# Performance work log

Hardware: AMD Instinct MI355X
Metric: run time of the kernel (lower is better)

Reference implementation:

```python
import jax, jax.numpy as jnp
import numpy as np

N_NODES = 100000
N_EDGES = 1600000
IN_CH = 128
OUT_CH = 64
HID = 2 * OUT_CH  # 128


def setup_inputs() -> dict:
    key = jax.random.key(0)
    ks = jax.random.split(key, 8)
    x = jax.random.normal(ks[0], (N_NODES, IN_CH), dtype=jnp.float32)
    edge_index = jax.random.randint(ks[1], (2, N_EDGES), 0, N_NODES, dtype=jnp.int64)

    def glorot(k, shape):
        return jax.random.normal(k, shape, dtype=jnp.float32) / jnp.sqrt(jnp.float32(shape[0]))

    W1 = glorot(ks[2], (IN_CH, HID))
    b1 = jax.random.normal(ks[3], (HID,), dtype=jnp.float32) * 0.01
    W_mu = glorot(ks[4], (HID, OUT_CH))
    b_mu = jax.random.normal(ks[5], (OUT_CH,), dtype=jnp.float32) * 0.01
    W_logstd = glorot(ks[6], (HID, OUT_CH))
    b_logstd = jax.random.normal(ks[7], (OUT_CH,), dtype=jnp.float32) * 0.01
    return {"x": x, "edge_index": edge_index, "W1": W1, "b1": b1,
            "W_mu": W_mu, "b_mu": b_mu, "W_logstd": W_logstd, "b_logstd": b_logstd}


def _gcn_norm(edge_index, n_nodes):
    # PyG GCNConv: add self-loops, symmetric normalization deg^{-1/2} A deg^{-1/2}
    loop = jnp.arange(n_nodes, dtype=edge_index.dtype)
    src = jnp.concatenate([edge_index[0], loop])  # [E+N]
    dst = jnp.concatenate([edge_index[1], loop])  # [E+N]
    deg = jax.ops.segment_sum(jnp.ones_like(dst, dtype=jnp.float32), dst,
                              num_segments=n_nodes)
    dinv = jnp.where(deg > 0, jax.lax.rsqrt(jnp.maximum(deg, 1.0)), 0.0)
    norm = dinv[src] * dinv[dst]  # [E+N]
    return src, dst, norm


def _gcn_conv(x, src, dst, norm, W, b, n_nodes):
    h = x @ W                                   # [N, out] linear first (small out dims)
    msg = h[src] * norm[:, None]                # [E+N, out] gather + scale
    out = jax.ops.segment_sum(msg, dst, num_segments=n_nodes)  # scatter-add
    return out + b


def reference(x, edge_index, W1, b1, W_mu, b_mu, W_logstd, b_logstd):
    n = x.shape[0]
    src, dst, norm = _gcn_norm(edge_index, n)  # same graph for all three layers
    h = jax.nn.relu(_gcn_conv(x, src, dst, norm, W1, b1, n))
    mu = _gcn_conv(h, src, dst, norm, W_mu, b_mu, n)
    logstd = _gcn_conv(h, src, dst, norm, W_logstd, b_logstd, n)
    return mu, logstd
```

## Files before the change

kernel.cpp:

```cpp
#include <hip/hip_runtime.h>
#include <stdint.h>

#define N_NODES 100000
#define N_EDGES 1600000
#define BSHIFT 9
#define NB 196
#define CAP 9216

typedef __attribute__((ext_vector_type(8))) short short8;
typedef __attribute__((ext_vector_type(4))) float f32x4;
typedef __attribute__((ext_vector_type(2))) float f32x2;
typedef __attribute__((ext_vector_type(4))) unsigned u32x4;
typedef __attribute__((ext_vector_type(2))) unsigned u32x2;
typedef __attribute__((ext_vector_type(4))) int i32x4;

static __device__ __forceinline__ unsigned short f2bf(float f){
  unsigned u = __float_as_uint(f);
  u += 0x7fffu + ((u >> 16) & 1u);
  return (unsigned short)(u >> 16);
}
static __device__ __forceinline__ unsigned pack2bf(float a, float b){
  return (unsigned)f2bf(a) | ((unsigned)f2bf(b) << 16);
}

__global__ __launch_bounds__(256)
void k_init(const float* __restrict__ W1, const float* __restrict__ Wmu,
            const float* __restrict__ Wls, short8* __restrict__ img,
            unsigned* __restrict__ gcur){
  int t = threadIdx.x;
  if (blockIdx.x == 16){
    if (t < NB) gcur[t] = t * CAP;
    return;
  }
  int gid = blockIdx.x*256 + t;
  int k = gid >> 11, slot = gid & 2047;
  int lane = slot & 63, ks = (slot >> 6) & 3, tt = slot >> 8;
  int c = tt*16 + (lane & 15);
  int kb = ks*32 + (lane >> 4)*8;
  short8 v;
  #pragma unroll
  for (int j = 0; j < 8; ++j){
    float f;
    if (k == 0) f = W1[(kb + j)*128 + c];
    else        f = (c < 64) ? Wmu[(kb + j)*64 + c] : Wls[(kb + j)*64 + (c - 64)];
    v[j] = (short)f2bf(f);
  }
  img[gid] = v;
}

__global__ __launch_bounds__(256)
void k_binB(const int* __restrict__ ei, unsigned* __restrict__ gcur,
            unsigned* __restrict__ tmp){
  __shared__ unsigned cnt[NB];
  __shared__ unsigned base[NB];
  int t = threadIdx.x;
  for (int j = t; j < NB; j += 256) cnt[j] = 0u;
  __syncthreads();
  unsigned bk[8], rk[8], en[8];
  int e0 = blockIdx.x*2048 + t*8;
  #pragma unroll
  for (int half = 0; half < 2; ++half){
    i32x4 sv, dv;
    bool any = (e0 + half*4) < N_EDGES;
    if (any){
      sv = *(const i32x4*)(ei + e0 + half*4);
      dv = *(const i32x4*)(ei + N_EDGES + e0 + half*4);
    }
    #pragma unroll
    for (int j = 0; j < 4; ++j){
      int q = half*4 + j;
      int e = e0 + q;
      bool ok = e < N_EDGES;
      unsigned d = ok ? (unsigned)dv[j] : 0u;
      unsigned s = ok ? (unsigned)sv[j] : 0u;
      ok = ok && d < N_NODES && s < N_NODES;
      bk[q] = ok ? (d >> BSHIFT) : 0xffffffffu;
      rk[q] = 0u; en[q] = 0u;
      if (ok){ rk[q] = atomicAdd(&cnt[bk[q]], 1u); en[q] = s | ((d & 511u) << 17); }
    }
  }
  __syncthreads();
  for (int j = t; j < NB; j += 256)
    base[j] = cnt[j] ? atomicAdd(&gcur[j], cnt[j]) : 0u;
  __syncthreads();
  #pragma unroll
  for (int j = 0; j < 8; ++j)
    if (bk[j] != 0xffffffffu){
      unsigned p = base[bk[j]] + rk[j];
      if (p < (bk[j] + 1u)*CAP) tmp[p] = en[j];
    }
}

__global__ __launch_bounds__(256)
void k_binC(const unsigned* __restrict__ gcur, const unsigned* __restrict__ tmp,
            unsigned* __restrict__ csr, unsigned* __restrict__ begdeg,
            float* __restrict__ dinv){
  __shared__ unsigned cnt[512];
  __shared__ unsigned cur[512];
  __shared__ unsigned sc[512];
  int b = blockIdx.x, t = threadIdx.x;
  unsigned base = (unsigned)b * CAP;
  unsigned sz = min(gcur[b] - base, (unsigned)CAP);
  cnt[t] = 0u; cnt[t + 256] = 0u;
  __syncthreads();
  for (unsigned idx = t; idx < sz; idx += 256){
    unsigned en = tmp[base + idx];
    atomicAdd(&cnt[(en >> 17) & 511u], 1u);
  }
  __syncthreads();
  sc[t] = cnt[t]; sc[t + 256] = cnt[t + 256];
  __syncthreads();
  for (int off = 1; off < 512; off <<= 1){
    unsigned a0 = (t >= off)       ? sc[t - off]       : 0u;
    unsigned a1 = (t + 256 >= off) ? sc[t + 256 - off] : 0u;
    __syncthreads();
    sc[t] += a0; sc[t + 256] += a1;
    __syncthreads();
  }
  {
    unsigned e0 = sc[t] - cnt[t], e1 = sc[t + 256] - cnt[t + 256];
    cur[t] = e0; cur[t + 256] = e1;
    int n0 = b*512 + t, n1 = b*512 + t + 256;
    if (n0 < N_NODES){
      begdeg[n0] = ((base + e0) << 11) | cnt[t];
      dinv[n0] = rsqrtf((float)(cnt[t] + 1u));
    }
    if (n1 < N_NODES){
      begdeg[n1] = ((base + e1) << 11) | cnt[t + 256];
      dinv[n1] = rsqrtf((float)(cnt[t + 256] + 1u));
    }
  }
  __syncthreads();
  for (unsigned idx = t; idx < sz; idx += 256){
    unsigned en = tmp[base + idx];
    unsigned p = atomicAdd(&cur[(en >> 17) & 511u], 1u);
    csr[base + p] = en;
  }
}

__global__ __launch_bounds__(256)
void k_pack(const unsigned* __restrict__ csr, const float* __restrict__ dinv,
            u32x2* __restrict__ csr2){
  int e = blockIdx.x*256 + threadIdx.x;
  if (e >= NB*CAP) return;
  unsigned src = csr[e] & 0x1FFFFu;
  src = min(src, (unsigned)(N_NODES - 1));
  u32x2 v; v[0] = src; v[1] = __float_as_uint(dinv[src]);
  csr2[e] = v;
}

template<bool AF32>
__global__ __launch_bounds__(256)
void k_gemm(const void* __restrict__ A_, const short8* __restrict__ img,
            unsigned short* __restrict__ out, int M)
{
  __shared__ short8 wf[2048];
  int tid = threadIdx.x;
  #pragma unroll
  for (int s = 0; s < 8; ++s) wf[tid + 256*s] = img[tid + 256*s];
  __syncthreads();

  int wave = tid >> 6, lane = tid & 63;
  int rb = blockIdx.x*128 + wave*32;
  int r0 = rb + (lane & 15);
  int r1 = r0 + 16;
  int ra0 = min(r0, M-1), ra1 = min(r1, M-1);
  int koff = (lane >> 4)*8;

  short8 a0[4], a1[4];
  if (AF32){
    const float* A = (const float*)A_;
    #pragma unroll
    for (int ks = 0; ks < 4; ++ks){
      const float* p0 = A + (size_t)ra0*128 + ks*32 + koff;
      const float* p1 = A + (size_t)ra1*128 + ks*32 + koff;
      f32x4 xa = *(const f32x4*)p0, xb = *(const f32x4*)(p0 + 4);
      f32x4 ya = *(const f32x4*)p1, yb = *(const f32x4*)(p1 + 4);
      short8 t0, t1;
      #pragma unroll
      for (int j = 0; j < 4; ++j){
        t0[j] = (short)f2bf(xa[j]); t0[j+4] = (short)f2bf(xb[j]);
        t1[j] = (short)f2bf(ya[j]); t1[j+4] = (short)f2bf(yb[j]);
      }
      a0[ks] = t0; a1[ks] = t1;
    }
  } else {
    const unsigned short* A = (const unsigned short*)A_;
    #pragma unroll
    for (int ks = 0; ks < 4; ++ks){
      a0[ks] = *(const short8*)(A + (size_t)ra0*128 + ks*32 + koff);
      a1[ks] = *(const short8*)(A + (size_t)ra1*128 + ks*32 + koff);
    }
  }

  f32x4 acc[2][8];
  #pragma unroll
  for (int t = 0; t < 8; ++t){ acc[0][t] = (f32x4)0.f; acc[1][t] = (f32x4)0.f; }

  #pragma unroll
  for (int t = 0; t < 8; ++t){
    #pragma unroll
    for (int ks = 0; ks < 4; ++ks){
      short8 b = wf[(t*4 + ks)*64 + lane];
      acc[0][t] = __builtin_amdgcn_mfma_f32_16x16x32_bf16(a0[ks], b, acc[0][t], 0, 0, 0);
      acc[1][t] = __builtin_amdgcn_mfma_f32_16x16x32_bf16(a1[ks], b, acc[1][t], 0, 0, 0);
    }
  }

  #pragma unroll
  for (int sub = 0; sub < 2; ++sub){
    int rbase = rb + sub*16 + (lane >> 4)*4;
    int c = lane & 15;
    #pragma unroll
    for (int t = 0; t < 8; ++t){
      #pragma unroll
      for (int j = 0; j < 4; ++j){
        int r = rbase + j;
        if (r < M) out[(size_t)r*128 + t*16 + c] = f2bf(acc[sub][t][j]);
      }
    }
  }
}

template<int MODE>
__global__ __launch_bounds__(256)
void k_agg(const unsigned short* __restrict__ hin, const unsigned* __restrict__ begdeg,
           const u32x2* __restrict__ csr2, const float* __restrict__ dinv,
           const float* __restrict__ bias, const float* __restrict__ bias2,
           unsigned* __restrict__ out_bf, float* __restrict__ out_f)
{
  int i = blockIdx.x*4 + (threadIdx.x >> 6);
  int lane = threadIdx.x & 63;
  int slot = lane >> 4, c8 = lane & 15;
  float di = dinv[i];

  f32x2 acc2[4];
  {
    u32x4 sv = *(const u32x4*)(hin + (size_t)i*128 + c8*8);
    float ws = (slot == 0) ? di*di : 0.f;
    #pragma unroll
    for (int j = 0; j < 4; ++j){
      f32x2 v; v.x = __uint_as_float(sv[j] << 16); v.y = __uint_as_float(sv[j] & 0xffff0000u);
      acc2[j].x = ws * v.x; acc2[j].y = ws * v.y;
    }
  }

  unsigned pk = begdeg[i];
  unsigned beg = pk >> 11, end = beg + (pk & 2047u);
  int nit = ((int)(pk & 2047u) + 7) >> 3;

  u32x2 fall; fall[0] = (unsigned)i; fall[1] = 0u;
  auto ldent = [&](int it, u32x2& e0, u32x2& e1){
    unsigned p0 = beg + (unsigned)(it*8) + (unsigned)(2*slot);
    unsigned p1 = p0 + 1;
    u32x2 t0 = csr2[p0 < end ? p0 : beg];
    u32x2 t1 = csr2[p1 < end ? p1 : beg];
    e0 = (p0 < end) ? t0 : fall;
    e1 = (p1 < end) ? t1 : fall;
  };

  u32x2 eA0, eA1, eB0, eB1;
  ldent(0, eA0, eA1);
  ldent(1, eB0, eB1);
  float    wA0 = di * __uint_as_float(eA0[1]), wA1 = di * __uint_as_float(eA1[1]);
  unsigned sA0 = eA0[0], sA1 = eA1[0];
  u32x4 rA0 = *(const u32x4*)(hin + (size_t)sA0*128 + c8*8);
  u32x4 rA1 = *(const u32x4*)(hin + (size_t)sA1*128 + c8*8);
  float    wB0 = di * __uint_as_float(eB0[1]), wB1 = di * __uint_as_float(eB1[1]);
  unsigned sB0 = eB0[0], sB1 = eB1[0];

  for (int it = 0; it < nit; ++it){
    u32x2 eC0, eC1;
    ldent(it + 2, eC0, eC1);
    u32x4 rB0 = *(const u32x4*)(hin + (size_t)sB0*128 + c8*8);
    u32x4 rB1 = *(const u32x4*)(hin + (size_t)sB1*128 + c8*8);

    f32x2 w0v; w0v.x = wA0; w0v.y = wA0;
    f32x2 w1v; w1v.x = wA1; w1v.y = wA1;
    #pragma unroll
    for (int j = 0; j < 4; ++j){
      f32x2 v0; v0.x = __uint_as_float(rA0[j] << 16); v0.y = __uint_as_float(rA0[j] & 0xffff0000u);
      f32x2 v1; v1.x = __uint_as_float(rA1[j] << 16); v1.y = __uint_as_float(rA1[j] & 0xffff0000u);
      acc2[j] = __builtin_elementwise_fma(w0v, v0, acc2[j]);
      acc2[j] = __builtin_elementwise_fma(w1v, v1, acc2[j]);
    }

    wA0 = wB0; wA1 = wB1; rA0 = rB0; rA1 = rB1;
    wB0 = di * __uint_as_float(eC0[1]); sB0 = eC0[0];
    wB1 = di * __uint_as_float(eC1[1]); sB1 = eC1[0];
  }

  #pragma unroll
  for (int j = 0; j < 4; ++j){
    acc2[j].x += __shfl_xor(acc2[j].x, 16);
    acc2[j].x += __shfl_xor(acc2[j].x, 32);
    acc2[j].y += __shfl_xor(acc2[j].y, 16);
    acc2[j].y += __shfl_xor(acc2[j].y, 32);
  }

  if (slot != 0) return;
  int c0 = c8*8;
  if (MODE == 0){
    u32x4 o;
    #pragma unroll
    for (int j = 0; j < 4; ++j){
      float lo = fmaxf(acc2[j].x + bias[c0 + 2*j],     0.f);
      float hi = fmaxf(acc2[j].y + bias[c0 + 2*j + 1], 0.f);
      o[j] = pack2bf(lo, hi);
    }
    *(u32x4*)(out_bf + (size_t)i*64 + c8*4) = o;
  } else {
    const float* bsrc = (c8 < 8) ? (bias + c0) : (bias2 + (c0 - 64));
    float* base = (c8 < 8) ? (out_f + (size_t)i*64 + c0)
                           : (out_f + (size_t)N_NODES*64 + (size_t)i*64 + (c0 - 64));
    f32x4 o0, o1;
    o0[0] = acc2[0].x + bsrc[0]; o0[1] = acc2[0].y + bsrc[1];
    o0[2] = acc2[1].x + bsrc[2]; o0[3] = acc2[1].y + bsrc[3];
    o1[0] = acc2[2].x + bsrc[4]; o1[1] = acc2[2].y + bsrc[5];
    o1[2] = acc2[3].x + bsrc[6]; o1[3] = acc2[3].y + bsrc[7];
    __builtin_nontemporal_store(o0, (f32x4*)base);
    __builtin_nontemporal_store(o1, (f32x4*)(base + 4));
  }
}


extern "C" void kernel_launch(void* const* d_in, const int* in_sizes, int n_in,
                              void* d_out, int out_size, void* d_ws, size_t ws_size,
                              hipStream_t stream)
{
  const float* x   = (const float*)d_in[0];
  const int*   ei  = (const int*)d_in[1];
  const float* W1  = (const float*)d_in[2];
  const float* b1  = (const float*)d_in[3];
  const float* Wmu = (const float*)d_in[4];
  const float* bmu = (const float*)d_in[5];
  const float* Wls = (const float*)d_in[6];
  const float* bls = (const float*)d_in[7];
  float* out = (float*)d_out;

  char* ws = (char*)d_ws;
  unsigned*       begdeg = (unsigned*)ws;        ws += 400128;
  float*          dinv   = (float*)ws;           ws += 400128;
  unsigned*       gcur   = (unsigned*)ws;        ws += 1024;
  short8*         imgW   = (short8*)ws;          ws += 65536;
  unsigned*       tmp    = (unsigned*)ws;        ws += 7225344;
  unsigned*       csr    = (unsigned*)ws;        ws += 7225344;
  u32x2*          csr2   = (u32x2*)ws;           ws += 14450688 + 256;
  unsigned short* bufA   = (unsigned short*)ws;  ws += 25600000;
  if (ws_size < (size_t)(ws - (char*)d_ws)) return;
  unsigned* bufB = (unsigned*)d_out;

  k_init<<<17, 256, 0, stream>>>(W1, Wmu, Wls, imgW, gcur);
  k_binB<<<(N_EDGES + 2047)/2048, 256, 0, stream>>>(ei, gcur, tmp);
  k_binC<<<NB, 256, 0, stream>>>(gcur, tmp, csr, begdeg, dinv);
  k_pack<<<(NB*CAP + 255)/256, 256, 0, stream>>>(csr, dinv, csr2);

  k_gemm<true ><<<(N_NODES + 127)/128, 256, 0, stream>>>(x, imgW, bufA, N_NODES);
  k_agg<0><<<N_NODES/4, 256, 0, stream>>>(bufA, begdeg, csr2, dinv, b1, nullptr,
                                          bufB, nullptr);
  k_gemm<false><<<(N_NODES + 127)/128, 256, 0, stream>>>((unsigned short*)bufB, imgW + 2048,
                                                         bufA, N_NODES);
  k_agg<1><<<N_NODES/4, 256, 0, stream>>>(bufA, begdeg, csr2, dinv, bmu, bls,
                                          nullptr, out);
}
```

Baseline: 218.9 us.

## Pad CSR rows to multiples of eight and stage bin scatter through LDS

Each node's CSR segment is padded to a multiple of 8 entries with zero-weight sentinel entries, so the aggregation kernel can read edge pairs as aligned 16-byte vector loads without bounds checks or fallback selects. In k_binB, edges are first grouped by bucket in shared memory with a local prefix scan, so the global scatter into tmp goes out in contiguous runs. The tmp buffer now shares memory with bufA to save workspace. The cost is a larger packed CSR (CAPP > CAP), padded entries that still gather row 0 with zero weight, and extra scan and sync work in the binning kernel.

Measured after the change: 220.1 us. No clear change (+0.6%).

```diff
diff --git a/kernel.cpp b/kernel.cpp
--- a/kernel.cpp
+++ b/kernel.cpp
@@ -5,7 +5,9 @@
 #define N_EDGES 1600000
 #define BSHIFT 9
 #define NB 196
-#define CAP 9216
+#define CAP_T 9216
+#define CAPP 11264
+#define SENT 0x80000000u
 
 typedef __attribute__((ext_vector_type(8))) short short8;
 typedef __attribute__((ext_vector_type(4))) float f32x4;
@@ -29,7 +31,7 @@
             unsigned* __restrict__ gcur){
   int t = threadIdx.x;
   if (blockIdx.x == 16){
-    if (t < NB) gcur[t] = t * CAP;
+    if (t < NB) gcur[t] = t * CAP_T;
     return;
   }
   int gid = blockIdx.x*256 + t;
@@ -52,7 +54,11 @@
 void k_binB(const int* __restrict__ ei, unsigned* __restrict__ gcur,
             unsigned* __restrict__ tmp){
   __shared__ unsigned cnt[NB];
-  __shared__ unsigned base[NB];
+  __shared__ unsigned gbase[NB];
+  __shared__ unsigned loff[NB];
+  __shared__ unsigned sc[256];
+  __shared__ unsigned sen[2048];
+  __shared__ unsigned spos[2048];
   int t = threadIdx.x;
   for (int j = t; j < NB; j += 256) cnt[j] = 0u;
   __syncthreads();
@@ -80,15 +86,33 @@
     }
   }
   __syncthreads();
-  for (int j = t; j < NB; j += 256)
-    base[j] = cnt[j] ? atomicAdd(&gcur[j], cnt[j]) : 0u;
-  __syncthreads();
+  sc[t] = (t < NB) ? cnt[t] : 0u;
+  __syncthreads();
+  for (int off = 1; off < 256; off <<= 1){
+    unsigned a = (t >= off) ? sc[t - off] : 0u;
+    __syncthreads();
+    sc[t] += a;
+    __syncthreads();
+  }
+  if (t < NB){
+    loff[t]  = sc[t] - cnt[t];
+    gbase[t] = cnt[t] ? atomicAdd(&gcur[t], cnt[t]) : 0u;
+  }
+  __syncthreads();
+  unsigned total = sc[NB - 1];
   #pragma unroll
   for (int j = 0; j < 8; ++j)
     if (bk[j] != 0xffffffffu){
-      unsigned p = base[bk[j]] + rk[j];
-      if (p < (bk[j] + 1u)*CAP) tmp[p] = en[j];
-    }
+      unsigned lp = loff[bk[j]] + rk[j];
+      unsigned gp = gbase[bk[j]] + rk[j];
+      sen[lp]  = en[j];
+      spos[lp] = (gp < (bk[j] + 1u)*CAP_T) ? gp : 0xffffffffu;
+    }
+  __syncthreads();
+  for (unsigned idx = t; idx < total; idx += 256){
+    unsigned p = spos[idx];
+    if (p != 0xffffffffu) tmp[p] = sen[idx];
+  }
 }
 
 __global__ __launch_bounds__(256)
@@ -99,16 +123,17 @@
   __shared__ unsigned cur[512];
   __shared__ unsigned sc[512];
   int b = blockIdx.x, t = threadIdx.x;
-  unsigned base = (unsigned)b * CAP;
-  unsigned sz = min(gcur[b] - base, (unsigned)CAP);
+  unsigned base_t = (unsigned)b * CAP_T;
+  unsigned basep  = (unsigned)b * CAPP;
+  unsigned sz = min(gcur[b] - base_t, (unsigned)CAP_T);
   cnt[t] = 0u; cnt[t + 256] = 0u;
   __syncthreads();
-  for (unsigned idx = t; idx < sz; idx += 256){
-    unsigned en = tmp[base + idx];
-    atomicAdd(&cnt[(en >> 17) & 511u], 1u);
-  }
-  __syncthreads();
-  sc[t] = cnt[t]; sc[t + 256] = cnt[t + 256];
+  for (unsigned idx = t; idx < sz; idx += 256)
+    atomicAdd(&cnt[(tmp[base_t + idx] >> 17) & 511u], 1u);
+  __syncthreads();
+  unsigned c0 = cnt[t], c1 = cnt[t + 256];
+  unsigned p0 = (c0 + 7u) & ~7u, p1 = (c1 + 7u) & ~7u;
+  sc[t] = p0; sc[t + 256] = p1;
   __syncthreads();
   for (int off = 1; off < 512; off <<= 1){
     unsigned a0 = (t >= off)       ? sc[t - off]       : 0u;
@@ -117,35 +142,41 @@
     sc[t] += a0; sc[t + 256] += a1;
     __syncthreads();
   }
+  unsigned e0 = sc[t] - p0, e1 = sc[t + 256] - p1;
+  cur[t] = e0; cur[t + 256] = e1;
   {
-    unsigned e0 = sc[t] - cnt[t], e1 = sc[t + 256] - cnt[t + 256];
-    cur[t] = e0; cur[t + 256] = e1;
-    int n0 = b*512 + t, n1 = b*512 + t + 256;
+    int n0 = b*512 + t, n1 = n0 + 256;
     if (n0 < N_NODES){
-      begdeg[n0] = ((base + e0) << 11) | cnt[t];
-      dinv[n0] = rsqrtf((float)(cnt[t] + 1u));
+      begdeg[n0] = (((basep + e0) >> 3) << 11) | min(c0, 2047u);
+      dinv[n0] = rsqrtf((float)(c0 + 1u));
+      for (unsigned k = c0; k < p0; ++k) csr[basep + e0 + k] = SENT;
     }
     if (n1 < N_NODES){
-      begdeg[n1] = ((base + e1) << 11) | cnt[t + 256];
-      dinv[n1] = rsqrtf((float)(cnt[t + 256] + 1u));
+      begdeg[n1] = (((basep + e1) >> 3) << 11) | min(c1, 2047u);
+      dinv[n1] = rsqrtf((float)(c1 + 1u));
+      for (unsigned k = c1; k < p1; ++k) csr[basep + e1 + k] = SENT;
     }
   }
   __syncthreads();
   for (unsigned idx = t; idx < sz; idx += 256){
-    unsigned en = tmp[base + idx];
+    unsigned en = tmp[base_t + idx];
     unsigned p = atomicAdd(&cur[(en >> 17) & 511u], 1u);
-    csr[base + p] = en;
+    if (p < (unsigned)CAPP) csr[basep + p] = en;
   }
 }
 
 __global__ __launch_bounds__(256)
 void k_pack(const unsigned* __restrict__ csr, const float* __restrict__ dinv,
             u32x2* __restrict__ csr2){
-  int e = blockIdx.x*256 + threadIdx.x;
-  if (e >= NB*CAP) return;
-  unsigned src = csr[e] & 0x1FFFFu;
-  src = min(src, (unsigned)(N_NODES - 1));
-  u32x2 v; v[0] = src; v[1] = __float_as_uint(dinv[src]);
+  unsigned e = blockIdx.x*256 + threadIdx.x;
+  if (e >= (unsigned)NB*CAPP) return;
+  unsigned en = csr[e];
+  u32x2 v;
+  if (en & SENT){ v[0] = 0u; v[1] = 0u; }
+  else {
+    unsigned src = min(en & 0x1FFFFu, (unsigned)(N_NODES - 1));
+    v[0] = src; v[1] = __float_as_uint(dinv[src]);
+  }
   csr2[e] = v;
 }
 
@@ -240,43 +271,28 @@
     float ws = (slot == 0) ? di*di : 0.f;
     #pragma unroll
     for (int j = 0; j < 4; ++j){
-      f32x2 v; v.x = __uint_as_float(sv[j] << 16); v.y = __uint_as_float(sv[j] & 0xffff0000u);
-      acc2[j].x = ws * v.x; acc2[j].y = ws * v.y;
+      acc2[j].x = ws * __uint_as_float(sv[j] << 16);
+      acc2[j].y = ws * __uint_as_float(sv[j] & 0xffff0000u);
     }
   }
 
   unsigned pk = begdeg[i];
-  unsigned beg = pk >> 11, end = beg + (pk & 2047u);
+  unsigned beg = (pk >> 11) << 3;
   int nit = ((int)(pk & 2047u) + 7) >> 3;
 
-  u32x2 fall; fall[0] = (unsigned)i; fall[1] = 0u;
-  auto ldent = [&](int it, u32x2& e0, u32x2& e1){
-    unsigned p0 = beg + (unsigned)(it*8) + (unsigned)(2*slot);
-    unsigned p1 = p0 + 1;
-    u32x2 t0 = csr2[p0 < end ? p0 : beg];
-    u32x2 t1 = csr2[p1 < end ? p1 : beg];
-    e0 = (p0 < end) ? t0 : fall;
-    e1 = (p1 < end) ? t1 : fall;
-  };
-
-  u32x2 eA0, eA1, eB0, eB1;
-  ldent(0, eA0, eA1);
-  ldent(1, eB0, eB1);
-  float    wA0 = di * __uint_as_float(eA0[1]), wA1 = di * __uint_as_float(eA1[1]);
-  unsigned sA0 = eA0[0], sA1 = eA1[0];
-  u32x4 rA0 = *(const u32x4*)(hin + (size_t)sA0*128 + c8*8);
-  u32x4 rA1 = *(const u32x4*)(hin + (size_t)sA1*128 + c8*8);
-  float    wB0 = di * __uint_as_float(eB0[1]), wB1 = di * __uint_as_float(eB1[1]);
-  unsigned sB0 = eB0[0], sB1 = eB1[0];
+  const u32x4* ep = (const u32x4*)(csr2 + beg + 2*slot);
+  u32x4 eA = ep[0];
+  u32x4 eB = ep[4];
+  u32x4 rA0 = *(const u32x4*)(hin + (size_t)eA[0]*128 + c8*8);
+  u32x4 rA1 = *(const u32x4*)(hin + (size_t)eA[2]*128 + c8*8);
 
   for (int it = 0; it < nit; ++it){
-    u32x2 eC0, eC1;
-    ldent(it + 2, eC0, eC1);
-    u32x4 rB0 = *(const u32x4*)(hin + (size_t)sB0*128 + c8*8);
-    u32x4 rB1 = *(const u32x4*)(hin + (size_t)sB1*128 + c8*8);
-
-    f32x2 w0v; w0v.x = wA0; w0v.y = wA0;
-    f32x2 w1v; w1v.x = wA1; w1v.y = wA1;
+    u32x4 eC = ep[4*it + 8];
+    u32x4 rB0 = *(const u32x4*)(hin + (size_t)eB[0]*128 + c8*8);
+    u32x4 rB1 = *(const u32x4*)(hin + (size_t)eB[2]*128 + c8*8);
+
+    f32x2 w0v; w0v.x = di * __uint_as_float(eA[1]); w0v.y = w0v.x;
+    f32x2 w1v; w1v.x = di * __uint_as_float(eA[3]); w1v.y = w1v.x;
     #pragma unroll
     for (int j = 0; j < 4; ++j){
       f32x2 v0; v0.x = __uint_as_float(rA0[j] << 16); v0.y = __uint_as_float(rA0[j] & 0xffff0000u);
@@ -285,9 +301,7 @@
       acc2[j] = __builtin_elementwise_fma(w1v, v1, acc2[j]);
     }
 
-    wA0 = wB0; wA1 = wB1; rA0 = rB0; rA1 = rB1;
-    wB0 = di * __uint_as_float(eC0[1]); sB0 = eC0[0];
-    wB1 = di * __uint_as_float(eC1[1]); sB1 = eC1[0];
+    eA = eB; eB = eC; rA0 = rB0; rA1 = rB1;
   }
 
   #pragma unroll
@@ -339,21 +353,22 @@
   float* out = (float*)d_out;
 
   char* ws = (char*)d_ws;
-  unsigned*       begdeg = (unsigned*)ws;        ws += 400128;
-  float*          dinv   = (float*)ws;           ws += 400128;
-  unsigned*       gcur   = (unsigned*)ws;        ws += 1024;
-  short8*         imgW   = (short8*)ws;          ws += 65536;
-  unsigned*       tmp    = (unsigned*)ws;        ws += 7225344;
-  unsigned*       csr    = (unsigned*)ws;        ws += 7225344;
-  u32x2*          csr2   = (u32x2*)ws;           ws += 14450688 + 256;
-  unsigned short* bufA   = (unsigned short*)ws;  ws += 25600000;
+  unsigned* begdeg = (unsigned*)ws;  ws += 400128;
+  float*    dinv   = (float*)ws;     ws += 400128;
+  unsigned* gcur   = (unsigned*)ws;  ws += 1024;
+  short8*   imgW   = (short8*)ws;    ws += 65536;
+  unsigned* csr    = (unsigned*)ws;  ws += (size_t)NB*CAPP*4;
+  u32x2*    csr2   = (u32x2*)ws;     ws += (size_t)NB*CAPP*8 + 512;
+  char*     shared = ws;             ws += 25600000;
   if (ws_size < (size_t)(ws - (char*)d_ws)) return;
+  unsigned*       tmp  = (unsigned*)shared;
+  unsigned short* bufA = (unsigned short*)shared;
   unsigned* bufB = (unsigned*)d_out;
 
   k_init<<<17, 256, 0, stream>>>(W1, Wmu, Wls, imgW, gcur);
   k_binB<<<(N_EDGES + 2047)/2048, 256, 0, stream>>>(ei, gcur, tmp);
   k_binC<<<NB, 256, 0, stream>>>(gcur, tmp, csr, begdeg, dinv);
-  k_pack<<<(NB*CAP + 255)/256, 256, 0, stream>>>(csr, dinv, csr2);
+  k_pack<<<(NB*CAPP + 255)/256, 256, 0, stream>>>(csr, dinv, csr2);
 
   k_gemm<true ><<<(N_NODES + 127)/128, 256, 0, stream>>>(x, imgW, bufA, N_NODES);
   k_agg<0><<<N_NODES/4, 256, 0, stream>>>(bufA, begdeg, csr2, dinv, b1, nullptr,
```
